# Kernel optimization log

Measured on AMD Instinct MI355X. Metric: run time of the kernel, lower is better.

The kernel has to match this reference:

```python
import jax, jax.numpy as jnp
import numpy as np

B, N, D_IN, D_OUT = 4, 2048, 1024, 1024


def setup_inputs() -> dict:
    key = jax.random.key(0)
    k0, k1, k2, k3 = jax.random.split(key, 4)
    x = jax.random.normal(k0, (B, N, D_IN), dtype=jnp.float32)
    # torch Linear weight is [out, in]; store transposed [in, out] for x @ W
    W_query = jax.random.normal(k1, (D_IN, D_OUT), dtype=jnp.float32) * (D_IN ** -0.5)
    W_key = jax.random.normal(k2, (D_IN, D_OUT), dtype=jnp.float32) * (D_IN ** -0.5)
    W_value = jax.random.normal(k3, (D_IN, D_OUT), dtype=jnp.float32) * (D_IN ** -0.5)
    return {"x": x, "W_query": W_query, "W_key": W_key, "W_value": W_value}


def reference(x, W_query, W_key, W_value):
    # x: [B, N, D_IN]
    num_tokens = x.shape[1]
    embed_dim = x.shape[2]  # NB: original scales by INPUT embed dim
    q = jnp.einsum('bnd,de->bne', x, W_query)  # [B, N, D_OUT]
    k = jnp.einsum('bnd,de->bne', x, W_key)
    v = jnp.einsum('bnd,de->bne', x, W_value)
    scores = jnp.einsum('bqe,bke->bqk', q, k)  # [B, N, N]
    idx = jnp.arange(num_tokens)
    causal_mask = idx[None, :] > idx[:, None]  # True above diagonal
    scores = jnp.where(causal_mask[None, :, :], -jnp.inf, scores)
    scale = jnp.asarray(embed_dim, scores.dtype) ** 0.5
    attn = jax.nn.softmax(scores / scale, axis=-1)  # dropout p=0 (eval)
    context = jnp.einsum('bqk,bke->bqe', attn, v)  # [B, N, D_OUT]
    return context
```

## Files before the change

### kernel.cpp

```cpp
#include <hip/hip_runtime.h>


typedef __attribute__((ext_vector_type(8))) _Float16 half8;
typedef __attribute__((ext_vector_type(4))) _Float16 half4v;
typedef __attribute__((ext_vector_type(4))) float floatx4;

#define AS1 __attribute__((address_space(1)))
#define AS3 __attribute__((address_space(3)))

__device__ __forceinline__ void load16_lds(void* lds, const void* g) {
  __builtin_amdgcn_global_load_lds((AS1 void*)g, (AS3 void*)lds, 16, 0, 0);
}


__global__ __launch_bounds__(256)
void conv_f32_f16(const float* __restrict__ in, _Float16* __restrict__ out,
                  float* __restrict__ l) {
  if (blockIdx.x < 8192) {
    const int i = (blockIdx.x * 256 + threadIdx.x) << 2;
    float4 v = *(const float4*)(in + i);
    half4v o = { (_Float16)v.x, (_Float16)v.y, (_Float16)v.z, (_Float16)v.w };
    *(half4v*)(out + i) = o;
  } else {
    const int i = ((blockIdx.x - 8192) * 256 + threadIdx.x) << 2;
    *(float4*)(l + i) = float4{0.f, 0.f, 0.f, 0.f};
  }
}

__global__ __launch_bounds__(256)
void transpose_w(const float* __restrict__ W0, const float* __restrict__ W1,
                 const float* __restrict__ W2, _Float16* __restrict__ Wt) {
  const float* W = blockIdx.z == 0 ? W0 : (blockIdx.z == 1 ? W1 : W2);
  _Float16* out = Wt + (long long)blockIdx.z * 1048576;
  __shared__ _Float16 t[32][33];
  const int tx = threadIdx.x, ty = threadIdx.y;
  const int n0 = blockIdx.x << 5, k0 = blockIdx.y << 5;
#pragma unroll
  for (int i = 0; i < 4; ++i)
    t[ty + i * 8][tx] = (_Float16)W[(long long)(k0 + ty + i * 8) * 1024 + n0 + tx];
  __syncthreads();
#pragma unroll
  for (int i = 0; i < 4; ++i)
    out[(long long)(n0 + ty + i * 8) * 1024 + k0 + tx] = t[tx][ty + i * 8];
}

__global__ __launch_bounds__(256)
void gemm_qkv(const _Float16* __restrict__ A, const _Float16* __restrict__ B,
              _Float16* __restrict__ Q, _Float16* __restrict__ Kh,
              _Float16* __restrict__ Vt) {
  const int bm = blockIdx.y, bn = blockIdx.x;
  const _Float16* Ab = A + (long long)bm * 128 * 1024;
  const _Float16* Bb = B + (long long)bn * 128 * 1024;

  __shared__ _Float16 As[128][64];
  __shared__ _Float16 Bs[128][64];

  const int tid = threadIdx.x;
  const int wave = tid >> 6, lane = tid & 63;
  const int quad = lane >> 4, lr = lane & 15;
  const int wm = (wave >> 1) << 6, wn = (wave & 1) << 6;
  const int srow = lane >> 3;
  const int goff = ((lane & 7) ^ srow) << 3;

  floatx4 acc[4][4] = {};
  const _Float16* ga = Ab + (long long)(wave * 8 + srow) * 1024 + goff;
  const _Float16* gb = Bb + (long long)(wave * 8 + srow) * 1024 + goff;

  for (int k0 = 0; k0 < 1024; k0 += 64) {
    __syncthreads();
#pragma unroll
    for (int c = 0; c < 4; ++c) {
      load16_lds(&As[wave * 8 + 32 * c][0], ga + c * 32 * 1024);
      load16_lds(&Bs[wave * 8 + 32 * c][0], gb + c * 32 * 1024);
    }
    ga += 64; gb += 64;
    __syncthreads();

#pragma unroll
    for (int kk = 0; kk < 2; ++kk) {
      half8 af[4], bf[4];
#pragma unroll
      for (int i = 0; i < 4; ++i) {
        const int ra = wm + (i << 4) + lr;
        const int rb = wn + (i << 4) + lr;
        af[i] = *(const half8*)&As[ra][(((kk << 2) + quad) ^ (ra & 7)) << 3];
        bf[i] = *(const half8*)&Bs[rb][(((kk << 2) + quad) ^ (rb & 7)) << 3];
      }
#pragma unroll
      for (int i = 0; i < 4; ++i)
#pragma unroll
        for (int j = 0; j < 4; ++j)
          acc[i][j] = __builtin_amdgcn_mfma_f32_16x16x32_f16(af[i], bf[j], acc[i][j], 0, 0, 0);
    }
  }

  const int colb = bn * 128 + wn + lr;
  const int rowb = bm * 128 + wm + (quad << 2);

  if (bn < 16) {
    _Float16* C = (bn < 8) ? Q : Kh;
    const int cb = colb & 1023;
#pragma unroll
    for (int i = 0; i < 4; ++i)
#pragma unroll
      for (int j = 0; j < 4; ++j)
#pragma unroll
        for (int r = 0; r < 4; ++r)
          C[(long long)(rowb + (i << 4) + r) * 1024 + cb + (j << 4)] =
              (_Float16)acc[i][j][r];
  } else {
    const int b = rowb >> 11;
    const int tb = rowb & 2047;
#pragma unroll
    for (int i = 0; i < 4; ++i) {
      const int tok = tb + (i << 4);
#pragma unroll
      for (int j = 0; j < 4; ++j) {
        const int d = (colb & 1023) + (j << 4);
        half4v v = { (_Float16)acc[i][j][0], (_Float16)acc[i][j][1],
                     (_Float16)acc[i][j][2], (_Float16)acc[i][j][3] };
        *(half4v*)&Vt[(long long)b * 2097152 + (long long)d * 2048 + tok] = v;
      }
    }
  }
}

__global__ __launch_bounds__(256)
void gemm_s_exp(const _Float16* __restrict__ Q, const _Float16* __restrict__ Kh,
                _Float16* __restrict__ P, float* __restrict__ l) {
  int t = blockIdx.x;
  const int bz = blockIdx.y;
  int bm = 0;
  for (;;) { const int c = (bm >> 2) + 1; if (t < c) break; t -= c; ++bm; }
  const int bn = t;

  const _Float16* Ab = Q  + (long long)bz * 2097152 + (long long)bm * 64 * 1024;
  const _Float16* Bb = Kh + (long long)bz * 2097152 + (long long)bn * 256 * 1024;
  const int nmaxl = bm * 64 + 63 - bn * 256;

  __shared__ _Float16 As[2][64][32];
  __shared__ _Float16 Bs[2][256][32];

  const int tid = threadIdx.x;
  const int wave = tid >> 6, lane = tid & 63;
  const int quad = lane >> 4, lr = lane & 15;
  const int srow = lane >> 2;
  const int goff = ((lane & 3) ^ ((srow >> 1) & 3)) << 3;

  const _Float16* ga = Ab + (long long)(16 * wave + srow) * 1024 + goff;
  const _Float16* gb = Bb + (long long)(64 * wave + srow) * 1024 + goff;

  floatx4 acc[4][4] = {};

  auto stage = [&](int buf, int kof) {
    load16_lds(&As[buf][16 * wave][0], ga + kof);
#pragma unroll
    for (int c = 0; c < 4; ++c)
      if (64 * wave + 16 * c <= nmaxl)
        load16_lds(&Bs[buf][64 * wave + 16 * c][0], gb + 16 * c * 1024 + kof);
  };

  stage(0, 0);
  for (int it = 0; it < 32; ++it) {
    __syncthreads();
    if (it + 1 < 32) stage((it + 1) & 1, (it + 1) * 32);
    const int buf = it & 1;

    half8 af[4], bf[4];
#pragma unroll
    for (int i = 0; i < 4; ++i) {
      const int ra = (i << 4) + lr;
      af[i] = *(const half8*)&As[buf][ra][(quad ^ ((ra >> 1) & 3)) << 3];
    }
#pragma unroll
    for (int j = 0; j < 4; ++j)
      if (64 * wave + (j << 4) <= nmaxl) {
        const int rb = 64 * wave + (j << 4) + lr;
        bf[j] = *(const half8*)&Bs[buf][rb][(quad ^ ((rb >> 1) & 3)) << 3];
      }
#pragma unroll
    for (int i = 0; i < 4; ++i)
#pragma unroll
      for (int j = 0; j < 4; ++j)
        if (64 * wave + (j << 4) <= nmaxl)
          acc[i][j] = __builtin_amdgcn_mfma_f32_16x16x32_f16(af[i], bf[j], acc[i][j], 0, 0, 0);
  }

  const int n0 = bn * 256 + wave * 64;
  const int rowq = bm * 64 + (quad << 2);
  _Float16* Pb = P + (long long)bz * 4194304;
  const float scl = 0.03125f;

  float rs[4][4];
#pragma unroll
  for (int i = 0; i < 4; ++i)
#pragma unroll
    for (int r = 0; r < 4; ++r) rs[i][r] = 0.f;

#pragma unroll
  for (int j = 0; j < 4; ++j)
    if (wave * 64 + (j << 4) <= nmaxl) {
      const int kcol = n0 + (j << 4) + lr;
#pragma unroll
      for (int i = 0; i < 4; ++i)
#pragma unroll
        for (int r = 0; r < 4; ++r) {
          const int q = rowq + (i << 4) + r;
          const float p = (kcol <= q) ? __expf(acc[i][j][r] * scl) : 0.f;
          Pb[(long long)q * 2048 + kcol] = (_Float16)p;
          rs[i][r] += p;
        }
    }

#pragma unroll
  for (int i = 0; i < 4; ++i)
#pragma unroll
    for (int r = 0; r < 4; ++r) {
#pragma unroll
      for (int off = 1; off < 16; off <<= 1)
        rs[i][r] += __shfl_xor(rs[i][r], off);
    }
  if (lr == 0) {
    float* lb = l + bz * 2048;
#pragma unroll
    for (int i = 0; i < 4; ++i)
#pragma unroll
      for (int r = 0; r < 4; ++r)
        atomicAdd(&lb[rowq + (i << 4) + r], rs[i][r]);
  }
}

__global__ __launch_bounds__(256)
void gemm_pv(const _Float16* __restrict__ P, const _Float16* __restrict__ Vt,
             const float* __restrict__ l, float* __restrict__ out) {
  const int bn = blockIdx.x, bz = blockIdx.z;
  const int bm = 31 - blockIdx.y;
  const int niter = 2 * (bm + 1);

  const _Float16* Ab = P  + (long long)bz * 4194304 + (long long)bm * 64 * 2048;
  const _Float16* Bb = Vt + (long long)bz * 2097152 + (long long)bn * 256 * 2048;

  __shared__ _Float16 As[2][64][32];
  __shared__ _Float16 Bs[2][256][32];

  const int tid = threadIdx.x;
  const int wave = tid >> 6, lane = tid & 63;
  const int quad = lane >> 4, lr = lane & 15;
  const int srow = lane >> 2;
  const int goff = ((lane & 3) ^ ((srow >> 1) & 3)) << 3;

  const _Float16* ga = Ab + (long long)(16 * wave + srow) * 2048 + goff;
  const _Float16* gb = Bb + (long long)(64 * wave + srow) * 2048 + goff;

  floatx4 acc[4][4] = {};

  auto stage = [&](int buf, int kof) {
    load16_lds(&As[buf][16 * wave][0], ga + kof);
#pragma unroll
    for (int c = 0; c < 4; ++c)
      load16_lds(&Bs[buf][64 * wave + 16 * c][0], gb + 16 * c * 2048 + kof);
  };

  stage(0, 0);
  for (int it = 0; it < niter; ++it) {
    __syncthreads();
    if (it + 1 < niter) stage((it + 1) & 1, (it + 1) * 32);
    const int buf = it & 1;

    half8 af[4], bf[4];
#pragma unroll
    for (int i = 0; i < 4; ++i) {
      const int ra = (i << 4) + lr;
      af[i] = *(const half8*)&As[buf][ra][(quad ^ ((ra >> 1) & 3)) << 3];
    }
#pragma unroll
    for (int j = 0; j < 4; ++j) {
      const int rb = 64 * wave + (j << 4) + lr;
      bf[j] = *(const half8*)&Bs[buf][rb][(quad ^ ((rb >> 1) & 3)) << 3];
    }
#pragma unroll
    for (int i = 0; i < 4; ++i)
#pragma unroll
      for (int j = 0; j < 4; ++j)
        acc[i][j] = __builtin_amdgcn_mfma_f32_16x16x32_f16(af[i], bf[j], acc[i][j], 0, 0, 0);
  }

  const int d0 = bn * 256 + wave * 64;
  const int rowq = bm * 64 + (quad << 2);
  const float* lb = l + bz * 2048;
  float* Cb = out + (long long)bz * 2097152;

  float linv[4][4];
#pragma unroll
  for (int i = 0; i < 4; ++i)
#pragma unroll
    for (int r = 0; r < 4; ++r)
      linv[i][r] = 1.0f / lb[rowq + (i << 4) + r];

#pragma unroll
  for (int i = 0; i < 4; ++i)
#pragma unroll
    for (int j = 0; j < 4; ++j)
#pragma unroll
      for (int r = 0; r < 4; ++r)
        Cb[(long long)(rowq + (i << 4) + r) * 1024 + d0 + (j << 4) + lr] =
            acc[i][j][r] * linv[i][r];
}


extern "C" void kernel_launch(void* const* d_in, const int* in_sizes, int n_in,
                              void* d_out, int out_size, void* d_ws, size_t ws_size,
                              hipStream_t stream) {
  const float* x  = (const float*)d_in[0];
  const float* Wq = (const float*)d_in[1];
  const float* Wk = (const float*)d_in[2];
  const float* Wv = (const float*)d_in[3];
  float* out = (float*)d_out;

  char* ws = (char*)d_ws;
  _Float16* xh = (_Float16*)(ws);
  _Float16* Wt = (_Float16*)(ws + 16777216);
  _Float16* Q  = (_Float16*)(ws + 23068672);
  _Float16* Kh = (_Float16*)(ws + 39845888);
  _Float16* Vt = (_Float16*)(ws + 56623104);
  _Float16* P  = (_Float16*)(ws + 73400320);
  float*    l  = (float*)   (ws + 106954752);

  conv_f32_f16<<<8200, 256, 0, stream>>>(x, xh, l);
  transpose_w<<<dim3(32, 32, 3), dim3(32, 8), 0, stream>>>(Wq, Wk, Wv, Wt);

  gemm_qkv<<<dim3(24, 64), 256, 0, stream>>>(xh, Wt, Q, Kh, Vt);

  gemm_s_exp<<<dim3(144, 4), 256, 0, stream>>>(Q, Kh, P, l);

  gemm_pv<<<dim3(4, 32, 4), 256, 0, stream>>>(P, Vt, l, out);
}
```

Baseline: 270.3 us.

## Replace LDS-staged score and PV GEMMs with direct-from-global streaming MFMA kernels

Both attention GEMMs (QK^T with exp, and PV) drop LDS double-buffering and now load MFMA fragments straight from global memory into registers. Tiles shrink from 64 to 32 query rows, which doubles the block count. The score kernel's triangular tiling changes to 256-wide key strips, which drops the per-wave skipping of masked fragments. The aim is to remove LDS staging and barrier overhead and to raise parallelism, at the cost of more redundant global/L2 traffic and poorly coalesced fragment loads.

```diff
diff --git a/kernel.cpp b/kernel.cpp
--- a/kernel.cpp
+++ b/kernel.cpp
@@ -126,94 +126,66 @@
 }
 
 __global__ __launch_bounds__(256)
-void gemm_s_exp(const _Float16* __restrict__ Q, const _Float16* __restrict__ Kh,
-                _Float16* __restrict__ P, float* __restrict__ l) {
+void s_exp_stream(const _Float16* __restrict__ Q, const _Float16* __restrict__ Kh,
+                  _Float16* __restrict__ P, float* __restrict__ l) {
   int t = blockIdx.x;
+  int s = 0;
+  for (;;) { const int c = 64 - 8 * s; if (t < c) break; t -= c; ++s; }
+  const int bm = 8 * s + t;
   const int bz = blockIdx.y;
-  int bm = 0;
-  for (;;) { const int c = (bm >> 2) + 1; if (t < c) break; t -= c; ++bm; }
-  const int bn = t;
-
-  const _Float16* Ab = Q  + (long long)bz * 2097152 + (long long)bm * 64 * 1024;
-  const _Float16* Bb = Kh + (long long)bz * 2097152 + (long long)bn * 256 * 1024;
-  const int nmaxl = bm * 64 + 63 - bn * 256;
-
-  __shared__ _Float16 As[2][64][32];
-  __shared__ _Float16 Bs[2][256][32];
+
+  const _Float16* Qb = Q  + (long long)bz * 2097152 + (long long)bm * 32 * 1024;
+  const _Float16* Kb = Kh + (long long)bz * 2097152 + (long long)s * 256 * 1024;
 
   const int tid = threadIdx.x;
   const int wave = tid >> 6, lane = tid & 63;
   const int quad = lane >> 4, lr = lane & 15;
-  const int srow = lane >> 2;
-  const int goff = ((lane & 3) ^ ((srow >> 1) & 3)) << 3;
-
-  const _Float16* ga = Ab + (long long)(16 * wave + srow) * 1024 + goff;
-  const _Float16* gb = Bb + (long long)(64 * wave + srow) * 1024 + goff;
-
-  floatx4 acc[4][4] = {};
-
-  auto stage = [&](int buf, int kof) {
-    load16_lds(&As[buf][16 * wave][0], ga + kof);
-#pragma unroll
-    for (int c = 0; c < 4; ++c)
-      if (64 * wave + 16 * c <= nmaxl)
-        load16_lds(&Bs[buf][64 * wave + 16 * c][0], gb + 16 * c * 1024 + kof);
-  };
-
-  stage(0, 0);
-  for (int it = 0; it < 32; ++it) {
-    __syncthreads();
-    if (it + 1 < 32) stage((it + 1) & 1, (it + 1) * 32);
-    const int buf = it & 1;
-
-    half8 af[4], bf[4];
-#pragma unroll
-    for (int i = 0; i < 4; ++i) {
-      const int ra = (i << 4) + lr;
-      af[i] = *(const half8*)&As[buf][ra][(quad ^ ((ra >> 1) & 3)) << 3];
-    }
-#pragma unroll
-    for (int j = 0; j < 4; ++j)
-      if (64 * wave + (j << 4) <= nmaxl) {
-        const int rb = 64 * wave + (j << 4) + lr;
-        bf[j] = *(const half8*)&Bs[buf][rb][(quad ^ ((rb >> 1) & 3)) << 3];
-      }
-#pragma unroll
-    for (int i = 0; i < 4; ++i)
+
+  const _Float16* ap = Qb + (long long)lr * 1024 + (quad << 3);
+  const _Float16* bp = Kb + (long long)(wave * 64 + lr) * 1024 + (quad << 3);
+
+  floatx4 acc[2][4] = {};
+#pragma unroll 2
+  for (int k0 = 0; k0 < 1024; k0 += 32) {
+    half8 af[2], bf[4];
+    af[0] = *(const half8*)(ap + k0);
+    af[1] = *(const half8*)(ap + 16 * 1024 + k0);
+#pragma unroll
+    for (int j = 0; j < 4; ++j)
+      bf[j] = *(const half8*)(bp + j * 16 * 1024 + k0);
+#pragma unroll
+    for (int i = 0; i < 2; ++i)
 #pragma unroll
       for (int j = 0; j < 4; ++j)
-        if (64 * wave + (j << 4) <= nmaxl)
-          acc[i][j] = __builtin_amdgcn_mfma_f32_16x16x32_f16(af[i], bf[j], acc[i][j], 0, 0, 0);
-  }
-
-  const int n0 = bn * 256 + wave * 64;
-  const int rowq = bm * 64 + (quad << 2);
+        acc[i][j] = __builtin_amdgcn_mfma_f32_16x16x32_f16(af[i], bf[j], acc[i][j], 0, 0, 0);
+  }
+
+  const int n0 = s * 256 + wave * 64;
+  const int q0 = bm * 32;
   _Float16* Pb = P + (long long)bz * 4194304;
   const float scl = 0.03125f;
 
-  float rs[4][4];
-#pragma unroll
-  for (int i = 0; i < 4; ++i)
+  float rs[2][4];
+#pragma unroll
+  for (int i = 0; i < 2; ++i)
 #pragma unroll
     for (int r = 0; r < 4; ++r) rs[i][r] = 0.f;
 
 #pragma unroll
-  for (int j = 0; j < 4; ++j)
-    if (wave * 64 + (j << 4) <= nmaxl) {
-      const int kcol = n0 + (j << 4) + lr;
-#pragma unroll
-      for (int i = 0; i < 4; ++i)
-#pragma unroll
-        for (int r = 0; r < 4; ++r) {
-          const int q = rowq + (i << 4) + r;
-          const float p = (kcol <= q) ? __expf(acc[i][j][r] * scl) : 0.f;
-          Pb[(long long)q * 2048 + kcol] = (_Float16)p;
-          rs[i][r] += p;
-        }
-    }
-
-#pragma unroll
-  for (int i = 0; i < 4; ++i)
+  for (int i = 0; i < 2; ++i)
+#pragma unroll
+    for (int j = 0; j < 4; ++j)
+#pragma unroll
+      for (int r = 0; r < 4; ++r) {
+        const int q = q0 + (i << 4) + (quad << 2) + r;
+        const int kcol = n0 + (j << 4) + lr;
+        const float p = (kcol <= q) ? __expf(acc[i][j][r] * scl) : 0.f;
+        Pb[(long long)q * 2048 + kcol] = (_Float16)p;
+        rs[i][r] += p;
+      }
+
+#pragma unroll
+  for (int i = 0; i < 2; ++i)
 #pragma unroll
     for (int r = 0; r < 4; ++r) {
 #pragma unroll
@@ -223,87 +195,66 @@
   if (lr == 0) {
     float* lb = l + bz * 2048;
 #pragma unroll
-    for (int i = 0; i < 4; ++i)
+    for (int i = 0; i < 2; ++i)
 #pragma unroll
       for (int r = 0; r < 4; ++r)
-        atomicAdd(&lb[rowq + (i << 4) + r], rs[i][r]);
-  }
-}
-
-__global__ __launch_bounds__(256)
-void gemm_pv(const _Float16* __restrict__ P, const _Float16* __restrict__ Vt,
-             const float* __restrict__ l, float* __restrict__ out) {
-  const int bn = blockIdx.x, bz = blockIdx.z;
-  const int bm = 31 - blockIdx.y;
-  const int niter = 2 * (bm + 1);
-
-  const _Float16* Ab = P  + (long long)bz * 4194304 + (long long)bm * 64 * 2048;
-  const _Float16* Bb = Vt + (long long)bz * 2097152 + (long long)bn * 256 * 2048;
-
-  __shared__ _Float16 As[2][64][32];
-  __shared__ _Float16 Bs[2][256][32];
+        atomicAdd(&lb[q0 + (i << 4) + (quad << 2) + r], rs[i][r]);
+  }
+}
+
+__global__ __launch_bounds__(256)
+void pv_stream(const _Float16* __restrict__ P, const _Float16* __restrict__ Vt,
+               const float* __restrict__ l, float* __restrict__ out) {
+  const int dn = blockIdx.x;
+  const int bm = 63 - blockIdx.y;
+  const int bz = blockIdx.z;
+  const int kmax = bm * 32 + 32;
+
+  const _Float16* Pb = P  + (long long)bz * 4194304 + (long long)bm * 32 * 2048;
+  const _Float16* Vb = Vt + (long long)bz * 2097152 + (long long)dn * 256 * 2048;
 
   const int tid = threadIdx.x;
   const int wave = tid >> 6, lane = tid & 63;
   const int quad = lane >> 4, lr = lane & 15;
-  const int srow = lane >> 2;
-  const int goff = ((lane & 3) ^ ((srow >> 1) & 3)) << 3;
-
-  const _Float16* ga = Ab + (long long)(16 * wave + srow) * 2048 + goff;
-  const _Float16* gb = Bb + (long long)(64 * wave + srow) * 2048 + goff;
-
-  floatx4 acc[4][4] = {};
-
-  auto stage = [&](int buf, int kof) {
-    load16_lds(&As[buf][16 * wave][0], ga + kof);
-#pragma unroll
-    for (int c = 0; c < 4; ++c)
-      load16_lds(&Bs[buf][64 * wave + 16 * c][0], gb + 16 * c * 2048 + kof);
-  };
-
-  stage(0, 0);
-  for (int it = 0; it < niter; ++it) {
-    __syncthreads();
-    if (it + 1 < niter) stage((it + 1) & 1, (it + 1) * 32);
-    const int buf = it & 1;
-
-    half8 af[4], bf[4];
-#pragma unroll
-    for (int i = 0; i < 4; ++i) {
-      const int ra = (i << 4) + lr;
-      af[i] = *(const half8*)&As[buf][ra][(quad ^ ((ra >> 1) & 3)) << 3];
-    }
-#pragma unroll
-    for (int j = 0; j < 4; ++j) {
-      const int rb = 64 * wave + (j << 4) + lr;
-      bf[j] = *(const half8*)&Bs[buf][rb][(quad ^ ((rb >> 1) & 3)) << 3];
-    }
-#pragma unroll
-    for (int i = 0; i < 4; ++i)
+
+  const _Float16* ap = Pb + (long long)lr * 2048 + (quad << 3);
+  const _Float16* bp = Vb + (long long)(wave * 64 + lr) * 2048 + (quad << 3);
+
+  floatx4 acc[2][4] = {};
+#pragma unroll 2
+  for (int k0 = 0; k0 < kmax; k0 += 32) {
+    half8 af[2], bf[4];
+    af[0] = *(const half8*)(ap + k0);
+    af[1] = *(const half8*)(ap + 16 * 2048 + k0);
+#pragma unroll
+    for (int j = 0; j < 4; ++j)
+      bf[j] = *(const half8*)(bp + j * 16 * 2048 + k0);
+#pragma unroll
+    for (int i = 0; i < 2; ++i)
 #pragma unroll
       for (int j = 0; j < 4; ++j)
         acc[i][j] = __builtin_amdgcn_mfma_f32_16x16x32_f16(af[i], bf[j], acc[i][j], 0, 0, 0);
   }
 
-  const int d0 = bn * 256 + wave * 64;
-  const int rowq = bm * 64 + (quad << 2);
+  const int d0 = dn * 256 + wave * 64;
+  const int q0 = bm * 32;
   const float* lb = l + bz * 2048;
   float* Cb = out + (long long)bz * 2097152;
 
-  float linv[4][4];
-#pragma unroll
-  for (int i = 0; i < 4; ++i)
+  float linv[2][4];
+#pragma unroll
+  for (int i = 0; i < 2; ++i)
 #pragma unroll
     for (int r = 0; r < 4; ++r)
-      linv[i][r] = 1.0f / lb[rowq + (i << 4) + r];
-
-#pragma unroll
-  for (int i = 0; i < 4; ++i)
+      linv[i][r] = 1.0f / lb[q0 + (i << 4) + (quad << 2) + r];
+
+#pragma unroll
+  for (int i = 0; i < 2; ++i)
 #pragma unroll
     for (int j = 0; j < 4; ++j)
 #pragma unroll
       for (int r = 0; r < 4; ++r)
-        Cb[(long long)(rowq + (i << 4) + r) * 1024 + d0 + (j << 4) + lr] =
+        Cb[(long long)(q0 + (i << 4) + (quad << 2) + r) * 1024 + d0 + (j << 4) + lr] =
             acc[i][j][r] * linv[i][r];
 }
 
@@ -331,7 +282,7 @@
 
   gemm_qkv<<<dim3(24, 64), 256, 0, stream>>>(xh, Wt, Q, Kh, Vt);
 
-  gemm_s_exp<<<dim3(144, 4), 256, 0, stream>>>(Q, Kh, P, l);
-
-  gemm_pv<<<dim3(4, 32, 4), 256, 0, stream>>>(P, Vt, l, out);
-}
+  s_exp_stream<<<dim3(288, 4), 256, 0, stream>>>(Q, Kh, P, l);
+
+  pv_stream<<<dim3(4, 64, 4), 256, 0, stream>>>(P, Vt, l, out);
+}
```

Result: slower. 431.7 us (+59.7%).
